# Optimization experiments

Hardware: AMD Instinct MI355X
Metric: run time of the kernel (lower is better)

The kernel has to match this reference:

```python
import jax, jax.numpy as jnp
import numpy as np

# Shapes: n groups, l = max group length, d = d_h, N = total queries (nq.sum()).
N_Q, N_GRP, L, D = 4096, 256, 64, 512


def setup_inputs() -> dict:
    key = jax.random.key(0)
    ks = jax.random.split(key, 8)
    q = jax.random.normal(ks[0], (N_Q, 2 * D), dtype=jnp.float32)      # cat([h_src, h_dst])
    k = jax.random.normal(ks[1], (N_GRP, L, D), dtype=jnp.float32)      # h_grp
    v = jax.random.normal(ks[2], (N_GRP, L, D), dtype=jnp.float32)      # x_grp
    m = (jax.random.uniform(ks[3], (N_GRP, L)) > 0.2).astype(jnp.float32)
    # sorted group id per query == repeat_interleave(arange(n), nq)
    gid = jnp.sort(jax.random.randint(ks[4], (N_Q,), 0, N_GRP))
    Wq = jax.random.normal(ks[5], (2 * D, D), dtype=jnp.float32) / np.float32(np.sqrt(2 * D))
    bq = jnp.zeros((D,), dtype=jnp.float32)
    Wk = jax.random.normal(ks[6], (D, D), dtype=jnp.float32) / np.float32(np.sqrt(D))
    bk = jnp.zeros((D,), dtype=jnp.float32)
    return dict(q=q, k=k, v=v, m=m, gid=gid, Wq=Wq, bq=bq, Wk=Wk, bk=bk)


def reference(q, k, v, m, gid, Wq, bq, Wk, bk):
    """Faithful jax version of NounPhraseModel.attention.

    torch: q -> self.q(q); k -> self.k(k); repeat_interleave(nq, 0) on k/v/m;
    s = (k @ q) / sqrt(d) - (exp(50*(1-m)) - 1); out = (v * softmax(s, 1)).sum(1).
    repeat_interleave is expressed as a gather by the per-query group id `gid`.
    """
    d = k.shape[-1]
    qp = q @ Wq + bq                                   # (N, d)   self.q(q)
    kp = k @ Wk + bk                                   # (n, l, d) self.k(k)
    kg = kp[gid]                                       # (N, l, d)
    vg = v[gid]                                        # (N, l, d)
    mg = m[gid]                                        # (N, l)
    s = jnp.einsum('nd,nld->nl', qp, kg) / jnp.sqrt(jnp.float32(d))
    s = s - (jnp.exp(50.0 * (1.0 - mg)) - 1.0)         # exponential mask bias
    a = jax.nn.softmax(s, axis=1)                      # softmax over group length
    return jnp.einsum('nl,nld->nd', a, vg)             # (N, d)
```

## Files before the change

kernel.cpp:

```cpp
#include <hip/hip_runtime.h>

#define NQ   4096
#define NGRP 256
#define LL   64
#define DD   512

typedef __attribute__((ext_vector_type(8))) short short8v;
typedef __attribute__((ext_vector_type(4))) float f32x4;
typedef __attribute__((ext_vector_type(4))) unsigned short us4v;

#define SCALE 0.044194173824159216f

static __device__ __forceinline__ unsigned short f2bf(float f) {
  union { float f; unsigned u; } x{f};
  unsigned r = x.u + 0x7fffu + ((x.u >> 16) & 1u);
  return (unsigned short)(r >> 16);
}
static __device__ __forceinline__ float bf2f(unsigned short h) {
  union { unsigned u; float f; } x{(unsigned)h << 16};
  return x.f;
}

static __device__ __forceinline__ void gload16(const void* g, void* lds_wave_base) {
  __builtin_amdgcn_global_load_lds(
      (const __attribute__((address_space(1))) void*)g,
      (__attribute__((address_space(3))) void*)lds_wave_base, 16, 0, 0);
}

static __device__ __forceinline__ void split_store(
    unsigned short* Hh, unsigned short* Hl, int r, int c4, float4 v) {
  int s = c4 >> 1, hf = c4 & 1;
  int base = (r * 8 + (s ^ (r & 7))) * 8 + hf * 4;
  unsigned short h0 = f2bf(v.x), h1 = f2bf(v.y), h2 = f2bf(v.z), h3 = f2bf(v.w);
  us4v hv = {h0, h1, h2, h3};
  us4v lv = {f2bf(v.x - bf2f(h0)), f2bf(v.y - bf2f(h1)),
             f2bf(v.z - bf2f(h2)), f2bf(v.w - bf2f(h3))};
  *(us4v*)(Hh + base) = hv;
  *(us4v*)(Hl + base) = lv;
}

static __device__ __forceinline__ short8v frag(const unsigned short* P, int r, int sl) {
  return *(const short8v*)(P + (r * 8 + (sl ^ (r & 7))) * 8);
}
static __device__ __forceinline__ short8v frag16(const unsigned short* P, int r, int sl) {
  return *(const short8v*)(P + (r * 16 + (sl ^ (r & 7))) * 8);
}

__global__ __launch_bounds__(256) void k_prep(
    const float* __restrict__ q_in, const int* __restrict__ gid,
    const float* __restrict__ Wk, const float* __restrict__ Wq,
    const float* __restrict__ bq,
    unsigned short* __restrict__ qbf, int* __restrict__ starts,
    float* __restrict__ b2, unsigned short* __restrict__ w2t) {
  __shared__ __align__(16) unsigned short lds[4 * 64 * 64];
  int b = blockIdx.x, t = threadIdx.x;
  if (b < 128) {
    unsigned short* Ah = lds;
    unsigned short* Al = lds + 4096;
    unsigned short* Bh = lds + 8192;
    unsigned short* Bl = lds + 12288;
    int lane = t & 63, wid = t >> 6;
    int wm = wid >> 1, wn = wid & 1;
    int n0 = (b & 15) * 64, m0 = (b >> 4) * 64;
    f32x4 acc[2][2];
    #pragma unroll
    for (int i = 0; i < 2; ++i)
      #pragma unroll
      for (int j = 0; j < 2; ++j) acc[i][j] = (f32x4){0.f,0.f,0.f,0.f};

    for (int k0 = 0; k0 < 512; k0 += 64) {
      __syncthreads();
      #pragma unroll
      for (int i = 0; i < 4; ++i) {
        int idx = i * 256 + t, r = idx >> 4, c4 = idx & 15;
        float4 vA = *(const float4*)&Wk[(size_t)(m0 + r) * 512 + k0 + c4 * 4];
        split_store(Ah, Al, r, c4, vA);
        float4 vB = *(const float4*)&Wq[(size_t)(n0 + r) * 512 + k0 + c4 * 4];
        split_store(Bh, Bl, r, c4, vB);
      }
      __syncthreads();
      #pragma unroll
      for (int kk = 0; kk < 2; ++kk) {
        int sl = kk * 4 + (lane >> 4);
        short8v aH[2], aL[2], bH[2], bL[2];
        #pragma unroll
        for (int fm = 0; fm < 2; ++fm) {
          int r = wm * 32 + fm * 16 + (lane & 15);
          aH[fm] = frag(Ah, r, sl); aL[fm] = frag(Al, r, sl);
        }
        #pragma unroll
        for (int fn = 0; fn < 2; ++fn) {
          int r = wn * 32 + fn * 16 + (lane & 15);
          bH[fn] = frag(Bh, r, sl); bL[fn] = frag(Bl, r, sl);
        }
        #pragma unroll
        for (int fm = 0; fm < 2; ++fm)
          #pragma unroll
          for (int fn = 0; fn < 2; ++fn) {
            acc[fm][fn] = __builtin_amdgcn_mfma_f32_16x16x32_bf16(aH[fm], bH[fn], acc[fm][fn], 0, 0, 0);
            acc[fm][fn] = __builtin_amdgcn_mfma_f32_16x16x32_bf16(aH[fm], bL[fn], acc[fm][fn], 0, 0, 0);
            acc[fm][fn] = __builtin_amdgcn_mfma_f32_16x16x32_bf16(aL[fm], bH[fn], acc[fm][fn], 0, 0, 0);
          }
      }
    }
    int cn = lane & 15, rq = lane >> 4;
    #pragma unroll
    for (int fm = 0; fm < 2; ++fm)
      #pragma unroll
      for (int fn = 0; fn < 2; ++fn)
        #pragma unroll
        for (int j = 0; j < 4; ++j) {
          int m = m0 + wm * 32 + fm * 16 + rq * 4 + j;
          int n = n0 + wn * 32 + fn * 16 + cn;
          w2t[(size_t)m * 1024 + n] = f2bf(acc[fm][fn][j]);
        }
  } else if (b < 2176) {
    int idx = (b - 128) * 256 + t;
    const float* src = q_in + (size_t)idx * 8;
    float4 f0 = *(const float4*)src;
    float4 f1 = *(const float4*)(src + 4);
    uint4 pk;
    pk.x = (unsigned)f2bf(f0.x) | ((unsigned)f2bf(f0.y) << 16);
    pk.y = (unsigned)f2bf(f0.z) | ((unsigned)f2bf(f0.w) << 16);
    pk.z = (unsigned)f2bf(f1.x) | ((unsigned)f2bf(f1.y) << 16);
    pk.w = (unsigned)f2bf(f1.z) | ((unsigned)f2bf(f1.w) << 16);
    ((uint4*)qbf)[idx] = pk;
  } else if (b == 2176) {
    for (int g = t; g <= NGRP; g += 256) {
      int lo = 0, hi = NQ;
      while (lo < hi) { int mid = (lo + hi) >> 1; if (gid[mid] < g) lo = mid + 1; else hi = mid; }
      starts[g] = lo;
    }
  } else {
    int dd = (b - 2177) * 256 + t;
    if (dd < DD) {
      float s = 0.f;
      const float* row = Wk + (size_t)dd * DD;
      for (int j = 0; j < DD; j += 4) {
        float4 w = *(const float4*)&row[j];
        float4 bb = *(const float4*)&bq[j];
        s += w.x*bb.x + w.y*bb.y + w.z*bb.z + w.w*bb.w;
      }
      b2[dd] = s;
    }
  }
}

__global__ __launch_bounds__(256) void gemm_qt_mfma(
    const unsigned short* __restrict__ qbf,
    const unsigned short* __restrict__ w2t,
    const float* __restrict__ b2,
    unsigned short* __restrict__ qt) {
  __shared__ __align__(16) unsigned short As[64 * 128];
  __shared__ __align__(16) unsigned short Bs[64 * 128];
  int t = threadIdx.x;
  int lane = t & 63, wid = t >> 6;
  int wm = wid >> 1, wn = wid & 1;
  int n0 = blockIdx.x * 64, m0 = blockIdx.y * 64;

  f32x4 acc[2][2];
  #pragma unroll
  for (int i = 0; i < 2; ++i)
    #pragma unroll
    for (int j = 0; j < 2; ++j) acc[i][j] = (f32x4){0.f, 0.f, 0.f, 0.f};

  for (int k0 = 0; k0 < 1024; k0 += 128) {
    __syncthreads();
    #pragma unroll
    for (int i = 0; i < 4; ++i) {
      int idx = i * 256 + t;
      int r = idx >> 4, ssw = idx & 15;
      int scol = ssw ^ (r & 7);
      gload16(qbf + (size_t)(m0 + r) * 1024 + k0 + scol * 8,
              (char*)As + (i * 256 + wid * 64) * 16);
      gload16(w2t + (size_t)(n0 + r) * 1024 + k0 + scol * 8,
              (char*)Bs + (i * 256 + wid * 64) * 16);
    }
    __syncthreads();
    #pragma unroll
    for (int kk = 0; kk < 4; ++kk) {
      short8v aF[2], bF[2];
      int sl = kk * 4 + (lane >> 4);
      #pragma unroll
      for (int fm = 0; fm < 2; ++fm)
        aF[fm] = frag16(As, wm * 32 + fm * 16 + (lane & 15), sl);
      #pragma unroll
      for (int fn = 0; fn < 2; ++fn)
        bF[fn] = frag16(Bs, wn * 32 + fn * 16 + (lane & 15), sl);
      #pragma unroll
      for (int fm = 0; fm < 2; ++fm)
        #pragma unroll
        for (int fn = 0; fn < 2; ++fn)
          acc[fm][fn] = __builtin_amdgcn_mfma_f32_16x16x32_bf16(aF[fm], bF[fn], acc[fm][fn], 0, 0, 0);
    }
  }
  int cn = lane & 15, rq = lane >> 4;
  #pragma unroll
  for (int fn = 0; fn < 2; ++fn) {
    int n = n0 + wn * 32 + fn * 16 + cn;
    float bias = b2[n];
    #pragma unroll
    for (int fm = 0; fm < 2; ++fm)
      #pragma unroll
      for (int j = 0; j < 4; ++j) {
        int m = m0 + wm * 32 + fm * 16 + rq * 4 + j;
        qt[(size_t)m * 512 + n] = f2bf(acc[fm][fn][j] + bias);
      }
  }
}

__global__ __launch_bounds__(256) void k_scores4(
    const unsigned short* __restrict__ qt,
    const float* __restrict__ kk_, const int* __restrict__ starts,
    float* __restrict__ s_part) {
  int g = blockIdx.x >> 2, dq = blockIdx.x & 3;
  int t = threadIdx.x, lane = t & 63, wl = t >> 6;
  int s0 = starts[g], s1 = starts[g + 1];
  if (s0 >= s1) return;

  __shared__ __align__(16) unsigned short Kh[64*64], Kl[64*64];
  __shared__ __align__(16) unsigned short Qs[32*64];

  float* sp = s_part + (size_t)dq * NQ * LL;

  for (int cs = s0; cs < s1; cs += 32) {
    int qc = min(32, s1 - cs);
    f32x4 acc[2];
    acc[0] = (f32x4){0.f,0.f,0.f,0.f};
    acc[1] = (f32x4){0.f,0.f,0.f,0.f};

    #pragma unroll
    for (int kt = 0; kt < 2; ++kt) {
      int k0 = dq * 128 + kt * 64;
      __syncthreads();
      #pragma unroll
      for (int i = 0; i < 4; ++i) {
        int idx = i * 256 + t, r = idx >> 4, c4 = idx & 15;
        float4 v = *(const float4*)&kk_[((size_t)g * LL + r) * DD + k0 + c4 * 4];
        split_store(Kh, Kl, r, c4, v);
      }
      {
        int r = t >> 3, ssw = t & 7;
        int scol = ssw ^ (r & 7);
        gload16(qt + (size_t)(cs + r) * DD + k0 + scol * 8,
                (char*)Qs + wl * 64 * 16);
      }
      __syncthreads();
      #pragma unroll
      for (int kk = 0; kk < 2; ++kk) {
        int sl = kk * 4 + (lane >> 4);
        int rA = wl * 16 + (lane & 15);
        short8v aH = frag(Kh, rA, sl), aL = frag(Kl, rA, sl);
        #pragma unroll
        for (int fn = 0; fn < 2; ++fn) {
          short8v bF = frag(Qs, fn * 16 + (lane & 15), sl);
          acc[fn] = __builtin_amdgcn_mfma_f32_16x16x32_bf16(aH, bF, acc[fn], 0, 0, 0);
          acc[fn] = __builtin_amdgcn_mfma_f32_16x16x32_bf16(aL, bF, acc[fn], 0, 0, 0);
        }
      }
    }
    {
      int cq = lane & 15, rq = lane >> 4;
      #pragma unroll
      for (int fn = 0; fn < 2; ++fn) {
        int q = fn * 16 + cq;
        if (q < qc) {
          float* row = sp + (size_t)(cs + q) * LL;
          #pragma unroll
          for (int j = 0; j < 4; ++j)
            row[wl * 16 + rq * 4 + j] = acc[fn][j];
        }
      }
    }
  }
}

__global__ __launch_bounds__(256) void k_pv2(
    const float* __restrict__ s_part, const float* __restrict__ vv_,
    const float* __restrict__ msk, const int* __restrict__ starts,
    float* __restrict__ out) {
  int g = blockIdx.x >> 1, dh = blockIdx.x & 1;
  int t = threadIdx.x, lane = t & 63, wid = t >> 6;
  int s0 = starts[g], s1 = starts[g + 1];
  if (s0 >= s1) return;

  __shared__ __align__(16) float S_lds[32][68];
  __shared__ float bias_lds[LL];
  if (t < LL) bias_lds[t] = __expf(50.0f * (1.0f - msk[g * LL + t])) - 1.0f;

  const float* vb = vv_ + (size_t)g * LL * DD + dh * 256 + lane * 4;

  for (int cs = s0; cs < s1; cs += 32) {
    int qc = min(32, s1 - cs);
    __syncthreads();
    #pragma unroll
    for (int i = 0; i < 2; ++i) {
      int f = i * 256 + t;
      int q = f >> 4, l4 = f & 15;
      const float* p = s_part + (size_t)(cs + q) * LL + l4 * 4;
      float4 a0 = *(const float4*)p;
      float4 a1 = *(const float4*)(p + (size_t)NQ * LL);
      float4 a2 = *(const float4*)(p + (size_t)2 * NQ * LL);
      float4 a3 = *(const float4*)(p + (size_t)3 * NQ * LL);
      float4 r;
      r.x = (a0.x + a1.x + a2.x + a3.x) * SCALE - bias_lds[l4 * 4 + 0];
      r.y = (a0.y + a1.y + a2.y + a3.y) * SCALE - bias_lds[l4 * 4 + 1];
      r.z = (a0.z + a1.z + a2.z + a3.z) * SCALE - bias_lds[l4 * 4 + 2];
      r.w = (a0.w + a1.w + a2.w + a3.w) * SCALE - bias_lds[l4 * 4 + 3];
      *(float4*)&S_lds[q][l4 * 4] = r;
    }
    __syncthreads();
    {
      int q = t >> 3, i = t & 7;
      float4 x0 = *(const float4*)&S_lds[q][i * 8];
      float4 x1 = *(const float4*)&S_lds[q][i * 8 + 4];
      float mx = fmaxf(fmaxf(fmaxf(x0.x, x0.y), fmaxf(x0.z, x0.w)),
                       fmaxf(fmaxf(x1.x, x1.y), fmaxf(x1.z, x1.w)));
      #pragma unroll
      for (int off = 1; off < 8; off <<= 1) mx = fmaxf(mx, __shfl_xor(mx, off, 8));
      float e0 = __expf(x0.x - mx), e1 = __expf(x0.y - mx);
      float e2 = __expf(x0.z - mx), e3 = __expf(x0.w - mx);
      float e4 = __expf(x1.x - mx), e5 = __expf(x1.y - mx);
      float e6 = __expf(x1.z - mx), e7 = __expf(x1.w - mx);
      float sum = ((e0 + e1) + (e2 + e3)) + ((e4 + e5) + (e6 + e7));
      #pragma unroll
      for (int off = 1; off < 8; off <<= 1) sum += __shfl_xor(sum, off, 8);
      float inv = 1.0f / sum;
      *(float4*)&S_lds[q][i * 8]     = make_float4(e0 * inv, e1 * inv, e2 * inv, e3 * inv);
      *(float4*)&S_lds[q][i * 8 + 4] = make_float4(e4 * inv, e5 * inv, e6 * inv, e7 * inv);
    }
    __syncthreads();
    {
      float o[8][4];
      #pragma unroll
      for (int u = 0; u < 8; ++u)
        #pragma unroll
        for (int e = 0; e < 4; ++e) o[u][e] = 0.f;
      for (int l0 = 0; l0 < LL; l0 += 4) {
        float a_[8][4];
        #pragma unroll
        for (int u = 0; u < 8; ++u) {
          float4 av = *(const float4*)&S_lds[wid * 8 + u][l0];
          a_[u][0] = av.x; a_[u][1] = av.y; a_[u][2] = av.z; a_[u][3] = av.w;
        }
        #pragma unroll
        for (int e = 0; e < 4; ++e) {
          float4 vv = *(const float4*)&vb[(size_t)(l0 + e) * DD];
          #pragma unroll
          for (int u = 0; u < 8; ++u) {
            o[u][0] += a_[u][e] * vv.x;
            o[u][1] += a_[u][e] * vv.y;
            o[u][2] += a_[u][e] * vv.z;
            o[u][3] += a_[u][e] * vv.w;
          }
        }
      }
      #pragma unroll
      for (int u = 0; u < 8; ++u) {
        int q = wid * 8 + u;
        if (q < qc) {
          *(float4*)&out[(size_t)(cs + q) * DD + dh * 256 + lane * 4] =
              make_float4(o[u][0], o[u][1], o[u][2], o[u][3]);
        }
      }
    }
  }
}

extern "C" void kernel_launch(void* const* d_in, const int* in_sizes, int n_in,
                              void* d_out, int out_size, void* d_ws, size_t ws_size,
                              hipStream_t stream) {
  const float* q_in = (const float*)d_in[0];
  const float* k_in = (const float*)d_in[1];
  const float* v_in = (const float*)d_in[2];
  const float* m_in = (const float*)d_in[3];
  const int*   gid  = (const int*)d_in[4];
  const float* Wq   = (const float*)d_in[5];
  const float* bq   = (const float*)d_in[6];
  const float* Wk   = (const float*)d_in[7];
  float* out = (float*)d_out;

  unsigned short* w2t = (unsigned short*)d_ws;
  unsigned short* qt  = w2t + 512 * 1024;
  unsigned short* qbf = qt + 4096 * 512;
  float* b2 = (float*)(qbf + 4096 * 1024);
  int* starts = (int*)(b2 + 512);
  float* s_part = (float*)(starts + 512);

  k_prep<<<2179, 256, 0, stream>>>(q_in, gid, Wk, Wq, bq, qbf, starts, b2, w2t);
  gemm_qt_mfma<<<dim3(8, 64), 256, 0, stream>>>(qbf, w2t, b2, qt);
  k_scores4<<<NGRP * 4, 256, 0, stream>>>(qt, k_in, starts, s_part);
  k_pv2<<<NGRP * 2, 256, 0, stream>>>(s_part, v_in, m_in, starts, out);
}
```

Measured before the change: 64.32 us.

## Pre-convert K to single bf16 in prep and stream it to LDS directly

Raw K is now converted to bf16 once, in extra blocks of the prep kernel. The scores kernel uses direct global-to-LDS loads of this bf16 copy. It no longer splits each fp32 K element into hi/lo bf16 pairs, so half the MFMAs and the per-block conversion work go away. The cost is a lower-precision K operand (single bf16 instead of hi+lo), an extra global write and read of the converted K buffer, and more prep blocks.

```diff
diff --git a/kernel.cpp b/kernel.cpp
--- a/kernel.cpp
+++ b/kernel.cpp
@@ -25,6 +25,15 @@
   __builtin_amdgcn_global_load_lds(
       (const __attribute__((address_space(1))) void*)g,
       (__attribute__((address_space(3))) void*)lds_wave_base, 16, 0, 0);
+}
+
+static __device__ __forceinline__ uint4 pack8(float4 f0, float4 f1) {
+  uint4 pk;
+  pk.x = (unsigned)f2bf(f0.x) | ((unsigned)f2bf(f0.y) << 16);
+  pk.y = (unsigned)f2bf(f0.z) | ((unsigned)f2bf(f0.w) << 16);
+  pk.z = (unsigned)f2bf(f1.x) | ((unsigned)f2bf(f1.y) << 16);
+  pk.w = (unsigned)f2bf(f1.z) | ((unsigned)f2bf(f1.w) << 16);
+  return pk;
 }
 
 static __device__ __forceinline__ void split_store(
@@ -47,10 +56,12 @@
 }
 
 __global__ __launch_bounds__(256) void k_prep(
-    const float* __restrict__ q_in, const int* __restrict__ gid,
+    const float* __restrict__ q_in, const float* __restrict__ k_in,
+    const int* __restrict__ gid,
     const float* __restrict__ Wk, const float* __restrict__ Wq,
     const float* __restrict__ bq,
-    unsigned short* __restrict__ qbf, int* __restrict__ starts,
+    unsigned short* __restrict__ qbf, unsigned short* __restrict__ kbf,
+    int* __restrict__ starts,
     float* __restrict__ b2, unsigned short* __restrict__ w2t) {
   __shared__ __align__(16) unsigned short lds[4 * 64 * 64];
   int b = blockIdx.x, t = threadIdx.x;
@@ -117,21 +128,14 @@
   } else if (b < 2176) {
     int idx = (b - 128) * 256 + t;
     const float* src = q_in + (size_t)idx * 8;
-    float4 f0 = *(const float4*)src;
-    float4 f1 = *(const float4*)(src + 4);
-    uint4 pk;
-    pk.x = (unsigned)f2bf(f0.x) | ((unsigned)f2bf(f0.y) << 16);
-    pk.y = (unsigned)f2bf(f0.z) | ((unsigned)f2bf(f0.w) << 16);
-    pk.z = (unsigned)f2bf(f1.x) | ((unsigned)f2bf(f1.y) << 16);
-    pk.w = (unsigned)f2bf(f1.z) | ((unsigned)f2bf(f1.w) << 16);
-    ((uint4*)qbf)[idx] = pk;
+    ((uint4*)qbf)[idx] = pack8(*(const float4*)src, *(const float4*)(src + 4));
   } else if (b == 2176) {
     for (int g = t; g <= NGRP; g += 256) {
       int lo = 0, hi = NQ;
       while (lo < hi) { int mid = (lo + hi) >> 1; if (gid[mid] < g) lo = mid + 1; else hi = mid; }
       starts[g] = lo;
     }
-  } else {
+  } else if (b < 2179) {
     int dd = (b - 2177) * 256 + t;
     if (dd < DD) {
       float s = 0.f;
@@ -143,6 +147,10 @@
       }
       b2[dd] = s;
     }
+  } else {
+    int idx = (b - 2179) * 256 + t;
+    const float* src = k_in + (size_t)idx * 8;
+    ((uint4*)kbf)[idx] = pack8(*(const float4*)src, *(const float4*)(src + 4));
   }
 }
 
@@ -211,14 +219,14 @@
 
 __global__ __launch_bounds__(256) void k_scores4(
     const unsigned short* __restrict__ qt,
-    const float* __restrict__ kk_, const int* __restrict__ starts,
+    const unsigned short* __restrict__ kbf, const int* __restrict__ starts,
     float* __restrict__ s_part) {
   int g = blockIdx.x >> 2, dq = blockIdx.x & 3;
   int t = threadIdx.x, lane = t & 63, wl = t >> 6;
   int s0 = starts[g], s1 = starts[g + 1];
   if (s0 >= s1) return;
 
-  __shared__ __align__(16) unsigned short Kh[64*64], Kl[64*64];
+  __shared__ __align__(16) unsigned short Ks[64*64];
   __shared__ __align__(16) unsigned short Qs[32*64];
 
   float* sp = s_part + (size_t)dq * NQ * LL;
@@ -234,10 +242,12 @@
       int k0 = dq * 128 + kt * 64;
       __syncthreads();
       #pragma unroll
-      for (int i = 0; i < 4; ++i) {
-        int idx = i * 256 + t, r = idx >> 4, c4 = idx & 15;
-        float4 v = *(const float4*)&kk_[((size_t)g * LL + r) * DD + k0 + c4 * 4];
-        split_store(Kh, Kl, r, c4, v);
+      for (int i = 0; i < 2; ++i) {
+        int idx = i * 256 + t;
+        int r = idx >> 3, ssw = idx & 7;
+        int scol = ssw ^ (r & 7);
+        gload16(kbf + ((size_t)g * LL + r) * DD + k0 + scol * 8,
+                (char*)Ks + (i * 256 + wl * 64) * 16);
       }
       {
         int r = t >> 3, ssw = t & 7;
@@ -249,13 +259,11 @@
       #pragma unroll
       for (int kk = 0; kk < 2; ++kk) {
         int sl = kk * 4 + (lane >> 4);
-        int rA = wl * 16 + (lane & 15);
-        short8v aH = frag(Kh, rA, sl), aL = frag(Kl, rA, sl);
+        short8v aF = frag(Ks, wl * 16 + (lane & 15), sl);
         #pragma unroll
         for (int fn = 0; fn < 2; ++fn) {
           short8v bF = frag(Qs, fn * 16 + (lane & 15), sl);
-          acc[fn] = __builtin_amdgcn_mfma_f32_16x16x32_bf16(aH, bF, acc[fn], 0, 0, 0);
-          acc[fn] = __builtin_amdgcn_mfma_f32_16x16x32_bf16(aL, bF, acc[fn], 0, 0, 0);
+          acc[fn] = __builtin_amdgcn_mfma_f32_16x16x32_bf16(aF, bF, acc[fn], 0, 0, 0);
         }
       }
     }
@@ -386,9 +394,11 @@
   float* b2 = (float*)(qbf + 4096 * 1024);
   int* starts = (int*)(b2 + 512);
   float* s_part = (float*)(starts + 512);
-
-  k_prep<<<2179, 256, 0, stream>>>(q_in, gid, Wk, Wq, bq, qbf, starts, b2, w2t);
+  unsigned short* kbf = (unsigned short*)(s_part + 4 * NQ * LL);
+
+  k_prep<<<6275, 256, 0, stream>>>(q_in, k_in, gid, Wk, Wq, bq,
+                                   qbf, kbf, starts, b2, w2t);
   gemm_qt_mfma<<<dim3(8, 64), 256, 0, stream>>>(qbf, w2t, b2, qt);
-  k_scores4<<<NGRP * 4, 256, 0, stream>>>(qt, k_in, starts, s_part);
+  k_scores4<<<NGRP * 4, 256, 0, stream>>>(qt, kbf, starts, s_part);
   k_pv2<<<NGRP * 2, 256, 0, stream>>>(s_part, v_in, m_in, starts, out);
 }
```

New measurement: 64.13 us. About the same (-0.3%).
